# Optimization experiments

Measured on AMD Instinct MI355X. Metric: run time of the kernel, lower is better.

Reference implementation:

```python
import jax, jax.numpy as jnp
import numpy as np
from jax import lax

N, C, M = 512, 81, 28
NMS_THRESH = 0.5
EPS = 1e-4


def setup_inputs() -> dict:
    key = jax.random.key(0)
    k1, k2, k3, k4 = jax.random.split(key, 4)
    return {
        "left_logits": jax.random.normal(k1, (N, C, M, M), dtype=jnp.float32),
        "right_logits": jax.random.normal(k2, (N, C, M, M), dtype=jnp.float32),
        "scores": jax.random.uniform(k3, (N,), dtype=jnp.float32),
        "labels": jax.random.randint(k4, (N,), 0, C),
    }


def mask_nms_keep(probs, scores, thresh):
    # probs: [N, M, M] float mask probabilities; greedy suppression in score order.
    n = probs.shape[0]
    order = jnp.argsort(-scores)
    P = probs[order].reshape(n, -1)                  # [N, M*M] sorted by score desc
    inter = P @ P.T                                   # pairwise sum(mask_i * mask_j)
    u = P.sum(-1)                                     # per-mask area (numerator mask only)
    iou = inter / (u[:, None] + EPS)                  # asymmetric IoU as in mask_iou()
    upper = jnp.triu(jnp.ones((n, n), dtype=bool), 1) # j > i

    def body(i, suppressed):
        sup_row = (~suppressed[i]) & upper[i] & (iou[i] >= thresh)
        return suppressed | sup_row

    suppressed = lax.fori_loop(0, n, body, jnp.zeros(n, dtype=bool))
    keep_sorted = ~suppressed
    # map back to original detection order
    return jnp.zeros(n, dtype=bool).at[order].set(keep_sorted)


def reference(left_logits, right_logits, scores, labels):
    idx = jnp.arange(left_logits.shape[0])
    # full-tensor sigmoid then per-class gather, as in the original module
    left_prob = jax.nn.sigmoid(left_logits)[idx, labels][:, None]    # [N,1,M,M]
    right_prob = jax.nn.sigmoid(right_logits)[idx, labels][:, None]  # [N,1,M,M]

    # filter_empty: both sides must have nonzero mask mass
    valid = (left_prob[:, 0].sum((-1, -2)) > 0) & (right_prob[:, 0].sum((-1, -2)) > 0)

    left_keep = mask_nms_keep(left_prob[:, 0], scores, NMS_THRESH)
    right_keep = mask_nms_keep(right_prob[:, 0], scores, NMS_THRESH)
    keep = valid & left_keep & right_keep  # intersection of left/right NMS keeps

    probs = jnp.stack([left_prob, right_prob], axis=0)  # [2,N,1,M,M]
    return probs, keep
```

## Files before the change

### kernel.cpp

```cpp
#include <hip/hip_runtime.h>
#include <math.h>

#define NDET 512
#define NCLS 81
#define MM   784
#define PROBS_ELEMS (2 * NDET * MM)
#define NMS_TH 0.5
#define EPS_D  1e-4
#define SD 114


__global__ __launch_bounds__(256) void k1_gather_sigmoid(
    const float* __restrict__ left, const float* __restrict__ right,
    const int* __restrict__ labels, float* __restrict__ out,
    double* __restrict__ u) {
  int b = blockIdx.x;
  int s = b >> 9;
  int n = b & 511;
  const float* src = (s == 0) ? left : right;
  int lab = labels[n];
  const float4* in4 = (const float4*)(src + ((size_t)n * NCLS + lab) * MM);
  float4* out4 = (float4*)(out + ((size_t)s * NDET + n) * MM);
  int t = threadIdx.x;
  double local = 0.0;
  if (t < MM / 4) {
    float4 v = in4[t];
    float4 r;
    r.x = 1.0f / (1.0f + expf(-v.x));
    r.y = 1.0f / (1.0f + expf(-v.y));
    r.z = 1.0f / (1.0f + expf(-v.z));
    r.w = 1.0f / (1.0f + expf(-v.w));
    out4[t] = r;
    local = (double)r.x + (double)r.y + (double)r.z + (double)r.w;
  }
  __shared__ double red[256];
  red[t] = local;
  __syncthreads();
  for (int st = 128; st > 0; st >>= 1) {
    if (t < st) red[t] += red[t + st];
    __syncthreads();
  }
  if (t == 0) u[s * NDET + n] = red[0];
}

__global__ __launch_bounds__(512) void k2_sort(
    const float* __restrict__ scores, int* __restrict__ order) {
  __shared__ float sk[NDET];
  __shared__ int   si[NDET];
  int t = threadIdx.x;
  sk[t] = scores[t];
  si[t] = t;
  __syncthreads();
  for (int k = 2; k <= NDET; k <<= 1) {
    for (int j = k >> 1; j > 0; j >>= 1) {
      int p = t ^ j;
      if (p > t) {
        bool dir = ((t & k) == 0);
        float sa = sk[t], sb = sk[p];
        int ia = si[t], ib = si[p];
        bool aBeforeB = (sa > sb) || (sa == sb && ia < ib);
        bool doSwap = dir ? (!aBeforeB) : aBeforeB;
        if (doSwap) { sk[t] = sb; si[t] = ib; sk[p] = sa; si[p] = ia; }
      }
      __syncthreads();
    }
  }
  order[t] = si[t];
}

__global__ __launch_bounds__(256) void k3_iou(
    const float* __restrict__ P,
    const double* __restrict__ u,
    const int* __restrict__ order,
    unsigned int* __restrict__ bits32) {
  int bi = blockIdx.x;
  int s = bi / 136;
  int tri = bi % 136;
  int ti = 0, rem = tri;
  while (rem >= 16 - ti) { rem -= 16 - ti; ti++; }
  int tj = ti + rem;

  __shared__ __align__(16) float As[32][SD];
  __shared__ __align__(16) float Bs[32][SD];
  __shared__ int oi[32], oj[32];
  __shared__ double den[32];

  int t = threadIdx.x;
  if (t < 32) {
    int r = order[ti * 32 + t];
    oi[t] = r;
    den[t] = u[s * NDET + r] + EPS_D;
    oj[t] = order[tj * 32 + t];
  }
  __syncthreads();

  const float* Pside = P + (size_t)s * NDET * MM;
  int cx = t & 15;
  int ry = t >> 4;
  double a00 = 0.0, a01 = 0.0, a10 = 0.0, a11 = 0.0;

  for (int kc = 0; kc < 7; kc++) {
    int k0 = kc * 112;
    for (int e = t; e < 32 * 112; e += 256) {
      int r = e / 112;
      int c = e - r * 112;
      As[r][c] = Pside[(size_t)oi[r] * MM + k0 + c];
      Bs[r][c] = Pside[(size_t)oj[r] * MM + k0 + c];
    }
    __syncthreads();
    for (int kp = 0; kp < 56; kp++) {
      float2 fa0 = *(const float2*)&As[ry][2 * kp];
      float2 fa1 = *(const float2*)&As[ry + 16][2 * kp];
      float2 fb0 = *(const float2*)&Bs[cx][2 * kp];
      float2 fb1 = *(const float2*)&Bs[cx + 16][2 * kp];
      a00 += (double)fa0.x * (double)fb0.x; a00 += (double)fa0.y * (double)fb0.y;
      a01 += (double)fa0.x * (double)fb1.x; a01 += (double)fa0.y * (double)fb1.y;
      a10 += (double)fa1.x * (double)fb0.x; a10 += (double)fa1.y * (double)fb0.y;
      a11 += (double)fa1.x * (double)fb1.x; a11 += (double)fa1.y * (double)fb1.y;
    }
    __syncthreads();
  }

  bool p00 = (a00 / den[ry]      >= NMS_TH);
  bool p01 = (a01 / den[ry]      >= NMS_TH);
  bool p10 = (a10 / den[ry + 16] >= NMS_TH);
  bool p11 = (a11 / den[ry + 16] >= NMS_TH);
  unsigned long long bl0 = __ballot(p00);
  unsigned long long bh0 = __ballot(p01);
  unsigned long long bl1 = __ballot(p10);
  unsigned long long bh1 = __ballot(p11);
  int q = ry & 3;
  if (cx == 0) {
    unsigned m0 = (unsigned)((bl0 >> (16 * q)) & 0xffffull) |
                  ((unsigned)((bh0 >> (16 * q)) & 0xffffull) << 16);
    unsigned m1 = (unsigned)((bl1 >> (16 * q)) & 0xffffull) |
                  ((unsigned)((bh1 >> (16 * q)) & 0xffffull) << 16);
    bits32[((size_t)s * NDET + ti * 32 + ry) * 16 + tj] = m0;
    bits32[((size_t)s * NDET + ti * 32 + ry + 16) * 16 + tj] = m1;
  }
}

__global__ __launch_bounds__(512) void k4_greedy(
    const unsigned long long* __restrict__ bits,
    const int* __restrict__ order,
    const double* __restrict__ u,
    float* __restrict__ outKeep) {
  __shared__ unsigned long long B[2 * NDET * 8];
  __shared__ unsigned char keepO[2 * NDET];
  int t = threadIdx.x;

  for (int e = t; e < 2 * NDET * 8; e += 512) {
    unsigned long long w = bits[e];
    int g = e & 7;
    int i = (e >> 3) & 511;
    int gi = i >> 6;
    if (g < gi) {
      w = 0ull;
    } else if (g == gi) {
      int li = i & 63;
      w = (li == 63) ? 0ull : (w & (~0ull << (li + 1)));
    }
    B[e] = w;
  }
  __syncthreads();

  int wv = t >> 6;
  int lane = t & 63;
  if (wv < 2) {
    int s = wv;
    const unsigned long long* Bside = B + (size_t)s * NDET * 8;
    unsigned long long S0 = 0, S1 = 0, S2 = 0, S3 = 0,
                       S4 = 0, S5 = 0, S6 = 0, S7 = 0;

#define GROUP(G, SG, ORS)                                              \
    for (int li = 0; li < 64; li++) {                                  \
      unsigned act = (unsigned)((SG >> li) & 1ull);                    \
      if (__builtin_amdgcn_readfirstlane(act) == 0) {                  \
        const unsigned long long* row = Bside + ((((G) << 6) | li) << 3); \
        ORS                                                            \
      }                                                                \
    }
    GROUP(0, S0, { S0 |= row[0]; S1 |= row[1]; S2 |= row[2]; S3 |= row[3];
                   S4 |= row[4]; S5 |= row[5]; S6 |= row[6]; S7 |= row[7]; })
    GROUP(1, S1, { S1 |= row[1]; S2 |= row[2]; S3 |= row[3];
                   S4 |= row[4]; S5 |= row[5]; S6 |= row[6]; S7 |= row[7]; })
    GROUP(2, S2, { S2 |= row[2]; S3 |= row[3];
                   S4 |= row[4]; S5 |= row[5]; S6 |= row[6]; S7 |= row[7]; })
    GROUP(3, S3, { S3 |= row[3];
                   S4 |= row[4]; S5 |= row[5]; S6 |= row[6]; S7 |= row[7]; })
    GROUP(4, S4, { S4 |= row[4]; S5 |= row[5]; S6 |= row[6]; S7 |= row[7]; })
    GROUP(5, S5, { S5 |= row[5]; S6 |= row[6]; S7 |= row[7]; })
    GROUP(6, S6, { S6 |= row[6]; S7 |= row[7]; })
    GROUP(7, S7, { S7 |= row[7]; })
#undef GROUP

    unsigned long long Sarr[8] = {S0, S1, S2, S3, S4, S5, S6, S7};
#pragma unroll
    for (int g = 0; g < 8; g++) {
      int c = (g << 6) | lane;
      keepO[s * NDET + order[c]] =
          (unsigned char)(((Sarr[g] >> lane) & 1ull) ^ 1ull);
    }
  }
  __syncthreads();

  if (t < NDET) {
    bool valid = (u[t] > 0.0) && (u[NDET + t] > 0.0);
    outKeep[t] = (valid && keepO[t] && keepO[NDET + t]) ? 1.0f : 0.0f;
  }
}

extern "C" void kernel_launch(void* const* d_in, const int* in_sizes, int n_in,
                              void* d_out, int out_size, void* d_ws, size_t ws_size,
                              hipStream_t stream) {
  const float* left   = (const float*)d_in[0];
  const float* right  = (const float*)d_in[1];
  const float* scores = (const float*)d_in[2];
  const int*   labels = (const int*)d_in[3];
  float* out = (float*)d_out;

  char* ws = (char*)d_ws;
  double* u                = (double*)(ws + 0);
  int* order               = (int*)(ws + 8192);
  unsigned int* bits32     = (unsigned int*)(ws + 16384);
  unsigned long long* bits = (unsigned long long*)(ws + 16384);

  k1_gather_sigmoid<<<1024, 256, 0, stream>>>(left, right, labels, out, u);
  k2_sort<<<1, 512, 0, stream>>>(scores, order);
  k3_iou<<<272, 256, 0, stream>>>(out, u, order, bits32);
  k4_greedy<<<1, 512, 0, stream>>>(bits, order, u, out + PROBS_ELEMS);
}
```

Before: 306.2 us.

## Fuse gather-sigmoid with score sort, use wave reductions and fp64 smem tiles

Merges the gather/sigmoid kernel and the bitonic sort into one launch, with an extra block doing the sort and each wavefront handling one mask using shuffle reductions instead of a shared-memory tree. This removes a kernel launch and lets the sort overlap the elementwise work. The IoU kernel now loads tiles with float4 and converts to double once when storing to LDS, so the inner loop no longer converts on every multiply. The cost is doubled LDS footprint per block (about 58 KB), which may lower occupancy.

```diff
diff --git a/kernel.cpp b/kernel.cpp
--- a/kernel.cpp
+++ b/kernel.cpp
@@ -7,65 +7,63 @@
 #define PROBS_ELEMS (2 * NDET * MM)
 #define NMS_TH 0.5
 #define EPS_D  1e-4
-#define SD 114
-
-
-__global__ __launch_bounds__(256) void k1_gather_sigmoid(
+#define SDD 114
+
+
+__global__ __launch_bounds__(256) void k12_fused(
     const float* __restrict__ left, const float* __restrict__ right,
-    const int* __restrict__ labels, float* __restrict__ out,
-    double* __restrict__ u) {
-  int b = blockIdx.x;
-  int s = b >> 9;
-  int n = b & 511;
+    const float* __restrict__ scores, const int* __restrict__ labels,
+    float* __restrict__ out, double* __restrict__ u, int* __restrict__ order) {
+  if (blockIdx.x == 256) {
+    __shared__ float sk[NDET];
+    __shared__ int   si[NDET];
+    int t = threadIdx.x;
+    for (int e = t; e < NDET; e += 256) { sk[e] = scores[e]; si[e] = e; }
+    __syncthreads();
+    for (int k = 2; k <= NDET; k <<= 1) {
+      for (int j = k >> 1; j > 0; j >>= 1) {
+        for (int e = t; e < NDET; e += 256) {
+          int p = e ^ j;
+          if (p > e) {
+            bool dir = ((e & k) == 0);
+            float sa = sk[e], sb = sk[p];
+            int ia = si[e], ib = si[p];
+            bool aBeforeB = (sa > sb) || (sa == sb && ia < ib);
+            bool doSwap = dir ? (!aBeforeB) : aBeforeB;
+            if (doSwap) { sk[e] = sb; si[e] = ib; sk[p] = sa; si[p] = ia; }
+          }
+        }
+        __syncthreads();
+      }
+    }
+    for (int e = t; e < NDET; e += 256) order[e] = si[e];
+    return;
+  }
+
+  int wv = threadIdx.x >> 6;
+  int lane = threadIdx.x & 63;
+  int m = (blockIdx.x << 2) | wv;
+  int s = m >> 9;
+  int n = m & 511;
   const float* src = (s == 0) ? left : right;
   int lab = labels[n];
   const float4* in4 = (const float4*)(src + ((size_t)n * NCLS + lab) * MM);
   float4* out4 = (float4*)(out + ((size_t)s * NDET + n) * MM);
-  int t = threadIdx.x;
   double local = 0.0;
-  if (t < MM / 4) {
-    float4 v = in4[t];
+  for (int i = lane; i < MM / 4; i += 64) {
+    float4 v = in4[i];
     float4 r;
     r.x = 1.0f / (1.0f + expf(-v.x));
     r.y = 1.0f / (1.0f + expf(-v.y));
     r.z = 1.0f / (1.0f + expf(-v.z));
     r.w = 1.0f / (1.0f + expf(-v.w));
-    out4[t] = r;
-    local = (double)r.x + (double)r.y + (double)r.z + (double)r.w;
-  }
-  __shared__ double red[256];
-  red[t] = local;
-  __syncthreads();
-  for (int st = 128; st > 0; st >>= 1) {
-    if (t < st) red[t] += red[t + st];
-    __syncthreads();
-  }
-  if (t == 0) u[s * NDET + n] = red[0];
-}
-
-__global__ __launch_bounds__(512) void k2_sort(
-    const float* __restrict__ scores, int* __restrict__ order) {
-  __shared__ float sk[NDET];
-  __shared__ int   si[NDET];
-  int t = threadIdx.x;
-  sk[t] = scores[t];
-  si[t] = t;
-  __syncthreads();
-  for (int k = 2; k <= NDET; k <<= 1) {
-    for (int j = k >> 1; j > 0; j >>= 1) {
-      int p = t ^ j;
-      if (p > t) {
-        bool dir = ((t & k) == 0);
-        float sa = sk[t], sb = sk[p];
-        int ia = si[t], ib = si[p];
-        bool aBeforeB = (sa > sb) || (sa == sb && ia < ib);
-        bool doSwap = dir ? (!aBeforeB) : aBeforeB;
-        if (doSwap) { sk[t] = sb; si[t] = ib; sk[p] = sa; si[p] = ia; }
-      }
-      __syncthreads();
-    }
-  }
-  order[t] = si[t];
+    out4[i] = r;
+    local += (double)r.x + (double)r.y + (double)r.z + (double)r.w;
+  }
+#pragma unroll
+  for (int off = 32; off > 0; off >>= 1)
+    local += __shfl_down(local, off, 64);
+  if (lane == 0) u[s * NDET + n] = local;
 }
 
 __global__ __launch_bounds__(256) void k3_iou(
@@ -80,8 +78,8 @@
   while (rem >= 16 - ti) { rem -= 16 - ti; ti++; }
   int tj = ti + rem;
 
-  __shared__ __align__(16) float As[32][SD];
-  __shared__ __align__(16) float Bs[32][SD];
+  __shared__ __align__(16) double Asd[32][SDD];
+  __shared__ __align__(16) double Bsd[32][SDD];
   __shared__ int oi[32], oj[32];
   __shared__ double den[32];
 
@@ -101,22 +99,30 @@
 
   for (int kc = 0; kc < 7; kc++) {
     int k0 = kc * 112;
-    for (int e = t; e < 32 * 112; e += 256) {
-      int r = e / 112;
-      int c = e - r * 112;
-      As[r][c] = Pside[(size_t)oi[r] * MM + k0 + c];
-      Bs[r][c] = Pside[(size_t)oj[r] * MM + k0 + c];
+    for (int e = t; e < 32 * 28; e += 256) {
+      int r = e / 28;
+      int c4 = e - r * 28;
+      float4 va = *(const float4*)&Pside[(size_t)oi[r] * MM + k0 + 4 * c4];
+      float4 vb = *(const float4*)&Pside[(size_t)oj[r] * MM + k0 + 4 * c4];
+      double2 a0; a0.x = (double)va.x; a0.y = (double)va.y;
+      double2 a1; a1.x = (double)va.z; a1.y = (double)va.w;
+      double2 b0; b0.x = (double)vb.x; b0.y = (double)vb.y;
+      double2 b1; b1.x = (double)vb.z; b1.y = (double)vb.w;
+      *(double2*)&Asd[r][4 * c4]     = a0;
+      *(double2*)&Asd[r][4 * c4 + 2] = a1;
+      *(double2*)&Bsd[r][4 * c4]     = b0;
+      *(double2*)&Bsd[r][4 * c4 + 2] = b1;
     }
     __syncthreads();
     for (int kp = 0; kp < 56; kp++) {
-      float2 fa0 = *(const float2*)&As[ry][2 * kp];
-      float2 fa1 = *(const float2*)&As[ry + 16][2 * kp];
-      float2 fb0 = *(const float2*)&Bs[cx][2 * kp];
-      float2 fb1 = *(const float2*)&Bs[cx + 16][2 * kp];
-      a00 += (double)fa0.x * (double)fb0.x; a00 += (double)fa0.y * (double)fb0.y;
-      a01 += (double)fa0.x * (double)fb1.x; a01 += (double)fa0.y * (double)fb1.y;
-      a10 += (double)fa1.x * (double)fb0.x; a10 += (double)fa1.y * (double)fb0.y;
-      a11 += (double)fa1.x * (double)fb1.x; a11 += (double)fa1.y * (double)fb1.y;
+      double2 fa0 = *(const double2*)&Asd[ry][2 * kp];
+      double2 fa1 = *(const double2*)&Asd[ry + 16][2 * kp];
+      double2 fb0 = *(const double2*)&Bsd[cx][2 * kp];
+      double2 fb1 = *(const double2*)&Bsd[cx + 16][2 * kp];
+      a00 += fa0.x * fb0.x; a00 += fa0.y * fb0.y;
+      a01 += fa0.x * fb1.x; a01 += fa0.y * fb1.y;
+      a10 += fa1.x * fb0.x; a10 += fa1.y * fb0.y;
+      a11 += fa1.x * fb1.x; a11 += fa1.y * fb1.y;
     }
     __syncthreads();
   }
@@ -225,8 +231,7 @@
   unsigned int* bits32     = (unsigned int*)(ws + 16384);
   unsigned long long* bits = (unsigned long long*)(ws + 16384);
 
-  k1_gather_sigmoid<<<1024, 256, 0, stream>>>(left, right, labels, out, u);
-  k2_sort<<<1, 512, 0, stream>>>(scores, order);
+  k12_fused<<<257, 256, 0, stream>>>(left, right, scores, labels, out, u, order);
   k3_iou<<<272, 256, 0, stream>>>(out, u, order, bits32);
   k4_greedy<<<1, 512, 0, stream>>>(bits, order, u, out + PROBS_ELEMS);
 }
```

Measured after the change: 292.7 us. -4.4%, faster.
